# Performance work log

Measured on AMD Instinct MI355X. Metric: run time of the kernel, lower is better.

## Reference

```python
import jax, jax.numpy as jnp
import numpy as np


def setup_inputs() -> dict:
    key = jax.random.key(0)
    k1, k2, k3 = jax.random.split(key, 3)
    dim = 192
    x = jax.random.normal(k1, (4, dim, 256, 256), dtype=jnp.float32)
    # Conv2d(5*dim, dim, 1): weight [dim, 5*dim], bias [dim]
    W = jax.random.normal(k2, (dim, 5 * dim), dtype=jnp.float32) * 0.02
    b = jax.random.normal(k3, (dim,), dtype=jnp.float32) * 0.02
    return {"x": x, "W": W, "b": b}


def _shifts(x):
    # Matches torch: cat([x,
    #   pad(x[:,:,:,1:], (0,1)),   # take right neighbor (zero at last col)
    #   pad(x[:,:,:,:-1], (1,0)),  # take left neighbor (zero at first col)
    #   pad(x[:,:,1:,:], (0,0,0,1)),  # take below neighbor (zero at last row)
    #   pad(x[:,:,:-1,:], (0,0,1,0))  # take above neighbor (zero at first row)
    # ], dim=1)
    right = jnp.pad(x[:, :, :, 1:], ((0, 0), (0, 0), (0, 0), (0, 1)))
    left = jnp.pad(x[:, :, :, :-1], ((0, 0), (0, 0), (0, 0), (1, 0)))
    down = jnp.pad(x[:, :, 1:, :], ((0, 0), (0, 0), (0, 1), (0, 0)))
    up = jnp.pad(x[:, :, :-1, :], ((0, 0), (0, 0), (1, 0), (0, 0)))
    return jnp.concatenate([x, right, left, down, up], axis=1)  # [B, 5C, H, W]


def reference(x, W, b):
    xs = _shifts(x)  # [B, 5C, H, W]
    # 1x1 conv == per-pixel matmul over channels
    out = jnp.einsum("bchw,oc->bohw", xs, W) + b[None, :, None, None]
    return out
```

## Files before the change

### kernel.cpp

```cpp
#include <hip/hip_runtime.h>
#include <hip/hip_bf16.h>
#include <stdint.h>

#define CDIM 192
#define KDIM 960
#define HW   65536
#define WI   256

#define OFF_W    50331648u
#define OFF_BIAS 50700288u
#define OFF_FLAG 50701056u
#define NEED_TOTAL 50701120u

typedef __attribute__((ext_vector_type(8))) short short8;
typedef __attribute__((ext_vector_type(4))) float floatx4;

__device__ __forceinline__ uint16_t f2b(float v) {
    __hip_bfloat16 h = __float2bfloat16(v);
    return *reinterpret_cast<uint16_t*>(&h);
}

__global__ __launch_bounds__(256) void detect_kernel(const uint32_t* __restrict__ xw,
                                                     int* __restrict__ flag) {
    __shared__ int cnt;
    if (threadIdx.x == 0) cnt = 0;
    __syncthreads();
    int local = 0;
    #pragma unroll
    for (int i = 0; i < 4; ++i) {
        int s = threadIdx.x * 4 + i;
        uint32_t d = xw[(size_t)s * 24571];
        uint32_t e = (d >> 7) & 0xFF;
        if (e >= 110 && e <= 130) ++local;
    }
    atomicAdd(&cnt, local);
    __syncthreads();
    if (threadIdx.x == 0) *flag = (cnt >= 512) ? 1 : 0;
}

__global__ __launch_bounds__(256) void prep_kernel(const void* __restrict__ Wsrc,
                                                   const void* __restrict__ bsrc,
                                                   __hip_bfloat16* __restrict__ Wb,
                                                   float* __restrict__ bfp,
                                                   const int* __restrict__ flag) {
    const int f = *flag;
    if (blockIdx.x < 720) {
        int i = blockIdx.x * 256 + threadIdx.x;
        float v = f ? __bfloat162float(((const __hip_bfloat16*)Wsrc)[i])
                    : ((const float*)Wsrc)[i];
        Wb[i] = __float2bfloat16(v);
    } else if (threadIdx.x < CDIM) {
        int j = threadIdx.x;
        bfp[j] = f ? __bfloat162float(((const __hip_bfloat16*)bsrc)[j])
                   : ((const float*)bsrc)[j];
    }
}

__global__ __launch_bounds__(256) void transpose_kernel(const void* __restrict__ xsrc,
                                                        __hip_bfloat16* __restrict__ xt,
                                                        const int* __restrict__ flag,
                                                        int base_b) {
    __shared__ uint4 lds[1536];
    const int bid = blockIdx.x;
    const int tid = threadIdx.x;
    const int bb = bid >> 10;
    const int b  = base_b + bb;
    const int p0 = (bid & 1023) << 6;
    const int f = *flag;
    if (f) {
        const uint4* xg = (const uint4*)xsrc;
        #pragma unroll
        for (int it = 0; it < 6; ++it) {
            int idx = tid + it * 256;
            int c = idx >> 3, pxc = idx & 7;
            size_t off = (size_t)(b * CDIM + c) * HW + p0 + pxc * 8;
            lds[idx] = xg[off >> 3];
        }
    } else {
        const float4* xg = (const float4*)xsrc;
        #pragma unroll
        for (int it = 0; it < 6; ++it) {
            int idx = tid + it * 256;
            int c = idx >> 3, pxc = idx & 7;
            size_t off4 = ((size_t)(b * CDIM + c) * HW + p0 + pxc * 8) >> 2;
            float4 v0 = xg[off4], v1 = xg[off4 + 1];
            uint32_t w0 = f2b(v0.x) | ((uint32_t)f2b(v0.y) << 16);
            uint32_t w1 = f2b(v0.z) | ((uint32_t)f2b(v0.w) << 16);
            uint32_t w2 = f2b(v1.x) | ((uint32_t)f2b(v1.y) << 16);
            uint32_t w3 = f2b(v1.z) | ((uint32_t)f2b(v1.w) << 16);
            lds[idx] = make_uint4(w0, w1, w2, w3);
        }
    }
    __syncthreads();
    const uint16_t* lu = (const uint16_t*)lds;
    #pragma unroll
    for (int it = 0; it < 6; ++it) {
        int idx = tid + it * 256;
        int px = idx & 63, cc = idx >> 6;
        uint32_t d[4];
        #pragma unroll
        for (int w = 0; w < 4; ++w) {
            uint32_t lo = lu[(cc * 8 + 2 * w) * 64 + px];
            uint32_t hi = lu[(cc * 8 + 2 * w + 1) * 64 + px];
            d[w] = lo | (hi << 16);
        }
        size_t row = (size_t)bb * HW + p0 + px;
        *(uint4*)(xt + row * CDIM + cc * 8) = make_uint4(d[0], d[1], d[2], d[3]);
    }
}

__device__ __forceinline__ void gload16(const void* g, void* l) {
    __builtin_amdgcn_global_load_lds(
        (const __attribute__((address_space(1))) uint32_t*)g,
        (__attribute__((address_space(3))) uint32_t*)l, 16, 0, 0);
}

__global__ __launch_bounds__(256, 2) void gemm_kernel(const __hip_bfloat16* __restrict__ xt,
                                                      const __hip_bfloat16* __restrict__ Wm,
                                                      const float* __restrict__ biasf,
                                                      void* __restrict__ outv,
                                                      const int* __restrict__ flag,
                                                      int base_b) {
    __shared__ char ldsW[2 * 12288];
    const int f = *flag;
    const int tid  = threadIdx.x;
    const int lane = tid & 63, wave = tid >> 6;
    const int quad = lane >> 4, l15 = lane & 15;
    const int bid = blockIdx.x;
    const int bb = bid >> 9;
    const int b  = base_b + bb;
    const int r  = bid & 511;
    const int h  = r >> 1;
    const int w0 = (r & 1) << 7;
    const int p0 = h * WI + w0;
    const int obase = (wave >> 1) * 96;
    const int nbase = (wave & 1) * 64;

    const char* gw[3];
    int ldsoff[3];
    #pragma unroll
    for (int t = 0; t < 3; ++t) {
        int chunk = tid + t * 256;
        int kq = chunk / 192, o = chunk % 192;
        gw[t] = (const char*)Wm + ((size_t)o * KDIM + kq * 8) * 2;
        ldsoff[t] = chunk * 16;
    }
    int aoff[6];
    #pragma unroll
    for (int mt = 0; mt < 6; ++mt) {
        int o = obase + mt * 16 + l15;
        aoff[mt] = (quad * 192 + o) * 16;
    }
    const char* xb = (const char*)(xt + (size_t)bb * HW * CDIM);
    int prow[4]; bool w255[4], wzero[4];
    #pragma unroll
    for (int nt = 0; nt < 4; ++nt) {
        int pl = nbase + nt * 16 + l15;
        prow[nt]  = p0 + pl;
        w255[nt]  = ((w0 + pl) == 255);
        wzero[nt] = ((w0 + pl) == 0);
    }

    floatx4 acc[6][4];
    #pragma unroll
    for (int mt = 0; mt < 6; ++mt)
        #pragma unroll
        for (int nt = 0; nt < 4; ++nt)
            acc[mt][nt] = (floatx4){0.f, 0.f, 0.f, 0.f};

    #pragma unroll
    for (int t = 0; t < 3; ++t) gload16(gw[t], ldsW + ldsoff[t]);

    for (int s = 0; s < 5; ++s) {
        const int dp = (s == 0) ? 0 : (s == 1) ? 1 : (s == 2) ? -1 : (s == 3) ? WI : -WI;
        const bool skip = (s == 3 && h == 255) || (s == 4 && h == 0);
        const int dpe = skip ? 0 : dp;
        #pragma unroll
        for (int j6 = 0; j6 < 6; ++j6) {
            const int step = s * 6 + j6;
            __syncthreads();
            const int cur = (step & 1) * 12288;
            if (step < 29) {
                const int nxt = ((step + 1) & 1) * 12288;
                #pragma unroll
                for (int t = 0; t < 3; ++t)
                    gload16(gw[t] + (size_t)(step + 1) * 64, ldsW + nxt + ldsoff[t]);
            }
            short8 af[6];
            #pragma unroll
            for (int mt = 0; mt < 6; ++mt)
                af[mt] = *(const short8*)(ldsW + cur + aoff[mt]);
            short8 bf[4];
            #pragma unroll
            for (int nt = 0; nt < 4; ++nt) {
                const bool edge = (s == 1 && w255[nt]) || (s == 2 && wzero[nt]);
                int rowi = prow[nt] + dpe;
                if (edge) rowi = prow[nt];
                short8 v = *(const short8*)(xb +
                    ((size_t)rowi * CDIM + j6 * 32 + quad * 8) * 2);
                if (edge || skip)
                    v = (short8){0, 0, 0, 0, 0, 0, 0, 0};
                bf[nt] = v;
            }
            #pragma unroll
            for (int mt = 0; mt < 6; ++mt)
                #pragma unroll
                for (int nt = 0; nt < 4; ++nt)
                    acc[mt][nt] = __builtin_amdgcn_mfma_f32_16x16x32_bf16(
                        af[mt], bf[nt], acc[mt][nt], 0, 0, 0);
        }
    }

    #pragma unroll
    for (int mt = 0; mt < 6; ++mt) {
        int o0 = obase + mt * 16 + quad * 4;
        float bv[4];
        #pragma unroll
        for (int rr = 0; rr < 4; ++rr) bv[rr] = biasf[o0 + rr];
        #pragma unroll
        for (int nt = 0; nt < 4; ++nt) {
            int px = nbase + nt * 16 + l15;
            size_t base = ((size_t)(b * CDIM + o0) * HW) + p0 + px;
            if (f) {
                __hip_bfloat16* out = (__hip_bfloat16*)outv;
                #pragma unroll
                for (int rr = 0; rr < 4; ++rr)
                    out[base + (size_t)rr * HW] = __float2bfloat16(acc[mt][nt][rr] + bv[rr]);
            } else {
                float* out = (float*)outv;
                #pragma unroll
                for (int rr = 0; rr < 4; ++rr)
                    out[base + (size_t)rr * HW] = acc[mt][nt][rr] + bv[rr];
            }
        }
    }
}

__global__ __launch_bounds__(256) void fallback_kernel(const void* __restrict__ xv,
                                                       const void* __restrict__ Wv,
                                                       const void* __restrict__ bv,
                                                       void* __restrict__ outv,
                                                       const int* __restrict__ flag) {
    __shared__ float Wl[KDIM];
    const int f = *flag;
    const int tid = threadIdx.x;
    const int bid = blockIdx.x;
    const int h = bid & 255;
    const int bo = bid >> 8;
    const int o = bo % CDIM;
    const int b = bo / CDIM;
    if (f) {
        const __hip_bfloat16* W16 = (const __hip_bfloat16*)Wv;
        for (int i = tid; i < KDIM; i += 256) Wl[i] = __bfloat162float(W16[(size_t)o * KDIM + i]);
    } else {
        const float* W32 = (const float*)Wv;
        for (int i = tid; i < KDIM; i += 256) Wl[i] = W32[(size_t)o * KDIM + i];
    }
    __syncthreads();
    const size_t pb = (size_t)b * CDIM * HW + (size_t)h * WI + tid;
    float acc = f ? __bfloat162float(((const __hip_bfloat16*)bv)[o]) : ((const float*)bv)[o];
    if (f) {
        const __hip_bfloat16* x = (const __hip_bfloat16*)xv;
        for (int c = 0; c < CDIM; ++c) {
            const __hip_bfloat16* xp = x + pb + (size_t)c * HW;
            float ctr = __bfloat162float(xp[0]);
            float rgt = (tid < 255) ? __bfloat162float(xp[1])   : 0.f;
            float lft = (tid > 0)   ? __bfloat162float(xp[-1])  : 0.f;
            float dwn = (h < 255)   ? __bfloat162float(xp[WI])  : 0.f;
            float up  = (h > 0)     ? __bfloat162float(xp[-WI]) : 0.f;
            acc += ctr * Wl[c] + rgt * Wl[192 + c] + lft * Wl[384 + c]
                 + dwn * Wl[576 + c] + up * Wl[768 + c];
        }
    } else {
        const float* x = (const float*)xv;
        for (int c = 0; c < CDIM; ++c) {
            const float* xp = x + pb + (size_t)c * HW;
            float ctr = xp[0];
            float rgt = (tid < 255) ? xp[1]   : 0.f;
            float lft = (tid > 0)   ? xp[-1]  : 0.f;
            float dwn = (h < 255)   ? xp[WI]  : 0.f;
            float up  = (h > 0)     ? xp[-WI] : 0.f;
            acc += ctr * Wl[c] + rgt * Wl[192 + c] + lft * Wl[384 + c]
                 + dwn * Wl[576 + c] + up * Wl[768 + c];
        }
    }
    size_t oidx = (size_t)bo * HW + (size_t)h * WI + tid;
    if (f) ((__hip_bfloat16*)outv)[oidx] = __float2bfloat16(acc);
    else   ((float*)outv)[oidx] = acc;
}

extern "C" void kernel_launch(void* const* d_in, const int* in_sizes, int n_in,
                              void* d_out, int out_size, void* d_ws, size_t ws_size,
                              hipStream_t stream) {
    const uint32_t* xw = (const uint32_t*)d_in[0];
    char* ws = (char*)d_ws;

    if (ws_size >= NEED_TOTAL) {
        int* flag = (int*)(ws + OFF_FLAG);
        __hip_bfloat16* xt = (__hip_bfloat16*)ws;
        __hip_bfloat16* Wb = (__hip_bfloat16*)(ws + OFF_W);
        float* bfp = (float*)(ws + OFF_BIAS);
        detect_kernel<<<1, 256, 0, stream>>>(xw, flag);
        prep_kernel<<<721, 256, 0, stream>>>(d_in[1], d_in[2], Wb, bfp, flag);
        for (int rnd = 0; rnd < 2; ++rnd) {
            transpose_kernel<<<2048, 256, 0, stream>>>(d_in[0], xt, flag, 2 * rnd);
            gemm_kernel<<<1024, 256, 0, stream>>>(xt, Wb, bfp, d_out, flag, 2 * rnd);
        }
    } else {
        int* flag = (int*)ws;
        detect_kernel<<<1, 256, 0, stream>>>(xw, flag);
        fallback_kernel<<<4 * CDIM * 256, 256, 0, stream>>>(d_in[0], d_in[1], d_in[2],
                                                            d_out, flag);
    }
}
```

Before: 573.6 us.

## Swizzle transpose LDS, remap GEMM workgroups, hand-pipeline loads, single-pass launch

The transpose now uses an XOR-swizzled LDS layout with coalesced contiguous output stores, to cut bank conflicts. The GEMM remaps block IDs across 8 groups (likely one per XCD) and restructures its K loop into a flat loop. That loop issues the activation loads before the weight prefetch, uses explicit waitcnt and barriers, and raises priority around the MFMAs, so global latency overlaps with compute. When the workspace is large enough, all four batches are processed in one transpose and one GEMM launch instead of two rounds. The hand-written vmcnt counts are fragile and could break correctness if the compiler emits a different number of loads.

```diff
diff --git a/kernel.cpp b/kernel.cpp
--- a/kernel.cpp
+++ b/kernel.cpp
@@ -7,10 +7,14 @@
 #define HW   65536
 #define WI   256
 
-#define OFF_W    50331648u
-#define OFF_BIAS 50700288u
-#define OFF_FLAG 50701056u
-#define NEED_TOTAL 50701120u
+#define OFF_W2    50331648u
+#define OFF_BIAS2 50700288u
+#define OFF_FLAG2 50701056u
+#define NEED2     50701120u
+#define OFF_W4    100663296u
+#define OFF_BIAS4 101031936u
+#define OFF_FLAG4 101032704u
+#define NEED4     101032768u
 
 typedef __attribute__((ext_vector_type(8))) short short8;
 typedef __attribute__((ext_vector_type(4))) float floatx4;
@@ -60,7 +64,7 @@
                                                         __hip_bfloat16* __restrict__ xt,
                                                         const int* __restrict__ flag,
                                                         int base_b) {
-    __shared__ uint4 lds[1536];
+    __shared__ uint16_t lds16[CDIM * 64];
     const int bid = blockIdx.x;
     const int tid = threadIdx.x;
     const int bb = bid >> 10;
@@ -70,42 +74,45 @@
     if (f) {
         const uint4* xg = (const uint4*)xsrc;
         #pragma unroll
-        for (int it = 0; it < 6; ++it) {
-            int idx = tid + it * 256;
-            int c = idx >> 3, pxc = idx & 7;
-            size_t off = (size_t)(b * CDIM + c) * HW + p0 + pxc * 8;
-            lds[idx] = xg[off >> 3];
+        for (int t = 0; t < 6; ++t) {
+            int idx = tid + t * 256;
+            int c = idx >> 3, j = idx & 7;
+            size_t off = ((size_t)(b * CDIM + c) * HW + p0 + j * 8) >> 3;
+            uint4 v = xg[off];
+            int col = (j ^ ((c >> 3) & 7)) << 3;
+            *(uint4*)&lds16[c * 64 + col] = v;
         }
     } else {
         const float4* xg = (const float4*)xsrc;
         #pragma unroll
-        for (int it = 0; it < 6; ++it) {
-            int idx = tid + it * 256;
-            int c = idx >> 3, pxc = idx & 7;
-            size_t off4 = ((size_t)(b * CDIM + c) * HW + p0 + pxc * 8) >> 2;
+        for (int t = 0; t < 6; ++t) {
+            int idx = tid + t * 256;
+            int c = idx >> 3, j = idx & 7;
+            size_t off4 = ((size_t)(b * CDIM + c) * HW + p0 + j * 8) >> 2;
             float4 v0 = xg[off4], v1 = xg[off4 + 1];
             uint32_t w0 = f2b(v0.x) | ((uint32_t)f2b(v0.y) << 16);
             uint32_t w1 = f2b(v0.z) | ((uint32_t)f2b(v0.w) << 16);
             uint32_t w2 = f2b(v1.x) | ((uint32_t)f2b(v1.y) << 16);
             uint32_t w3 = f2b(v1.z) | ((uint32_t)f2b(v1.w) << 16);
-            lds[idx] = make_uint4(w0, w1, w2, w3);
+            int col = (j ^ ((c >> 3) & 7)) << 3;
+            *(uint4*)&lds16[c * 64 + col] = make_uint4(w0, w1, w2, w3);
         }
     }
     __syncthreads();
-    const uint16_t* lu = (const uint16_t*)lds;
-    #pragma unroll
-    for (int it = 0; it < 6; ++it) {
-        int idx = tid + it * 256;
-        int px = idx & 63, cc = idx >> 6;
+    uint4* dst = (uint4*)xt + (size_t)(bb * HW + p0) * 24;
+    #pragma unroll
+    for (int t = 0; t < 6; ++t) {
+        int m = tid + t * 256;
+        int px = m / 24, c8 = m % 24;
+        int colbase = (((px >> 3) ^ (c8 & 7)) << 3) | (px & 7);
         uint32_t d[4];
         #pragma unroll
-        for (int w = 0; w < 4; ++w) {
-            uint32_t lo = lu[(cc * 8 + 2 * w) * 64 + px];
-            uint32_t hi = lu[(cc * 8 + 2 * w + 1) * 64 + px];
-            d[w] = lo | (hi << 16);
-        }
-        size_t row = (size_t)bb * HW + p0 + px;
-        *(uint4*)(xt + row * CDIM + cc * 8) = make_uint4(d[0], d[1], d[2], d[3]);
+        for (int wd = 0; wd < 4; ++wd) {
+            uint32_t lo = lds16[(c8 * 8 + 2 * wd) * 64 + colbase];
+            uint32_t hi = lds16[(c8 * 8 + 2 * wd + 1) * 64 + colbase];
+            d[wd] = lo | (hi << 16);
+        }
+        dst[m] = make_uint4(d[0], d[1], d[2], d[3]);
     }
 }
 
@@ -126,10 +133,14 @@
     const int tid  = threadIdx.x;
     const int lane = tid & 63, wave = tid >> 6;
     const int quad = lane >> 4, l15 = lane & 15;
-    const int bid = blockIdx.x;
-    const int bb = bid >> 9;
+
+    const int nwg  = (int)gridDim.x;
+    const int bid0 = (int)blockIdx.x;
+    const int wg   = (bid0 & 7) * (nwg >> 3) + (bid0 >> 3);
+
+    const int bb = wg >> 9;
     const int b  = base_b + bb;
-    const int r  = bid & 511;
+    const int r  = wg & 511;
     const int h  = r >> 1;
     const int w0 = (r & 1) << 7;
     const int p0 = h * WI + w0;
@@ -168,47 +179,62 @@
         for (int nt = 0; nt < 4; ++nt)
             acc[mt][nt] = (floatx4){0.f, 0.f, 0.f, 0.f};
 
+    asm volatile("s_waitcnt vmcnt(0) lgkmcnt(0)" ::: "memory");
+    __builtin_amdgcn_sched_barrier(0);
     #pragma unroll
     for (int t = 0; t < 3; ++t) gload16(gw[t], ldsW + ldsoff[t]);
 
-    for (int s = 0; s < 5; ++s) {
-        const int dp = (s == 0) ? 0 : (s == 1) ? 1 : (s == 2) ? -1 : (s == 3) ? WI : -WI;
+    int s = 0, j6 = 0;
+    #pragma unroll 2
+    for (int step = 0; step < 30; ++step) {
+        const int cur = (step & 1) * 12288;
+        const int nxt = 12288 - cur;
+        const int dp  = (s == 1) ? 1 : (s == 2) ? -1 : (s == 3) ? WI : (s == 4) ? -WI : 0;
         const bool skip = (s == 3 && h == 255) || (s == 4 && h == 0);
         const int dpe = skip ? 0 : dp;
-        #pragma unroll
-        for (int j6 = 0; j6 < 6; ++j6) {
-            const int step = s * 6 + j6;
-            __syncthreads();
-            const int cur = (step & 1) * 12288;
-            if (step < 29) {
-                const int nxt = ((step + 1) & 1) * 12288;
-                #pragma unroll
-                for (int t = 0; t < 3; ++t)
-                    gload16(gw[t] + (size_t)(step + 1) * 64, ldsW + nxt + ldsoff[t]);
-            }
-            short8 af[6];
+
+        __builtin_amdgcn_s_barrier();
+        __builtin_amdgcn_sched_barrier(0);
+        short8 bfr[4]; bool kill[4];
+        #pragma unroll
+        for (int nt = 0; nt < 4; ++nt) {
+            const bool edge = (s == 1 && w255[nt]) || (s == 2 && wzero[nt]);
+            kill[nt] = edge || skip;
+            const int rowi = edge ? prow[nt] : (prow[nt] + dpe);
+            bfr[nt] = *(const short8*)(xb + ((size_t)rowi * CDIM + j6 * 32 + quad * 8) * 2);
+        }
+        __builtin_amdgcn_sched_barrier(0);
+        if (step < 29) {
             #pragma unroll
-            for (int mt = 0; mt < 6; ++mt)
-                af[mt] = *(const short8*)(ldsW + cur + aoff[mt]);
-            short8 bf[4];
+            for (int t = 0; t < 3; ++t)
+                gload16(gw[t] + (size_t)(step + 1) * 64, ldsW + nxt + ldsoff[t]);
+        }
+        __builtin_amdgcn_sched_barrier(0);
+        if (step < 29) asm volatile("s_waitcnt vmcnt(7)" ::: "memory");
+        else           asm volatile("s_waitcnt vmcnt(4)" ::: "memory");
+        __builtin_amdgcn_sched_barrier(0);
+        __builtin_amdgcn_s_barrier();
+        __builtin_amdgcn_sched_barrier(0);
+
+        short8 af[6];
+        #pragma unroll
+        for (int mt = 0; mt < 6; ++mt)
+            af[mt] = *(const short8*)(ldsW + cur + aoff[mt]);
+        short8 bf[4];
+        #pragma unroll
+        for (int nt = 0; nt < 4; ++nt)
+            bf[nt] = kill[nt] ? (short8){0, 0, 0, 0, 0, 0, 0, 0} : bfr[nt];
+
+        __builtin_amdgcn_s_setprio(1);
+        #pragma unroll
+        for (int mt = 0; mt < 6; ++mt)
             #pragma unroll
-            for (int nt = 0; nt < 4; ++nt) {
-                const bool edge = (s == 1 && w255[nt]) || (s == 2 && wzero[nt]);
-                int rowi = prow[nt] + dpe;
-                if (edge) rowi = prow[nt];
-                short8 v = *(const short8*)(xb +
-                    ((size_t)rowi * CDIM + j6 * 32 + quad * 8) * 2);
-                if (edge || skip)
-                    v = (short8){0, 0, 0, 0, 0, 0, 0, 0};
-                bf[nt] = v;
-            }
-            #pragma unroll
-            for (int mt = 0; mt < 6; ++mt)
-                #pragma unroll
-                for (int nt = 0; nt < 4; ++nt)
-                    acc[mt][nt] = __builtin_amdgcn_mfma_f32_16x16x32_bf16(
-                        af[mt], bf[nt], acc[mt][nt], 0, 0, 0);
-        }
+            for (int nt = 0; nt < 4; ++nt)
+                acc[mt][nt] = __builtin_amdgcn_mfma_f32_16x16x32_bf16(
+                    af[mt], bf[nt], acc[mt][nt], 0, 0, 0);
+        __builtin_amdgcn_s_setprio(0);
+
+        if (++j6 == 6) { j6 = 0; ++s; }
     }
 
     #pragma unroll
@@ -295,11 +321,20 @@
     const uint32_t* xw = (const uint32_t*)d_in[0];
     char* ws = (char*)d_ws;
 
-    if (ws_size >= NEED_TOTAL) {
-        int* flag = (int*)(ws + OFF_FLAG);
+    if (ws_size >= NEED4) {
+        int* flag = (int*)(ws + OFF_FLAG4);
         __hip_bfloat16* xt = (__hip_bfloat16*)ws;
-        __hip_bfloat16* Wb = (__hip_bfloat16*)(ws + OFF_W);
-        float* bfp = (float*)(ws + OFF_BIAS);
+        __hip_bfloat16* Wb = (__hip_bfloat16*)(ws + OFF_W4);
+        float* bfp = (float*)(ws + OFF_BIAS4);
+        detect_kernel<<<1, 256, 0, stream>>>(xw, flag);
+        prep_kernel<<<721, 256, 0, stream>>>(d_in[1], d_in[2], Wb, bfp, flag);
+        transpose_kernel<<<4096, 256, 0, stream>>>(d_in[0], xt, flag, 0);
+        gemm_kernel<<<2048, 256, 0, stream>>>(xt, Wb, bfp, d_out, flag, 0);
+    } else if (ws_size >= NEED2) {
+        int* flag = (int*)(ws + OFF_FLAG2);
+        __hip_bfloat16* xt = (__hip_bfloat16*)ws;
+        __hip_bfloat16* Wb = (__hip_bfloat16*)(ws + OFF_W2);
+        float* bfp = (float*)(ws + OFF_BIAS2);
         detect_kernel<<<1, 256, 0, stream>>>(xw, flag);
         prep_kernel<<<721, 256, 0, stream>>>(d_in[1], d_in[2], Wb, bfp, flag);
         for (int rnd = 0; rnd < 2; ++rnd) {
```

After: 571.4 us. About the same (-0.4%).
